# Kernel tuning notes

Measured on AMD Instinct MI355X. Metric: run time of the kernel, lower is better.

Reference implementation:

```python
import jax, jax.numpy as jnp
import numpy as np

# Module config
T = 4.0          # distillation temperature (init arg)
NUM_BINS = 256   # number of unique quantized feature values present in the tensors
N, C, H, W = 64, 256, 32, 32
EPS = 1e-8


def setup_inputs() -> dict:
    key = jax.random.key(0)
    k1, k2 = jax.random.split(key)
    # Quantized features: integer-valued floats in [0, NUM_BINS). All 256 levels
    # appear w.h.p., so torch.unique(features).sort()[0] == arange(NUM_BINS).
    feat_s = jax.random.randint(k1, (N, C, H, W), 0, NUM_BINS).astype(jnp.float32)
    feat_t = jax.random.randint(k2, (N, C, H, W), 0, NUM_BINS).astype(jnp.float32)
    return {"feat_s": feat_s, "feat_t": feat_t}


def _feature_to_prob(features):
    # Replaces the original per-unique-value Python loop with one fused
    # scatter-add histogram. Values are exact integers, so equality-compare
    # counting == bincount on the integer cast.
    b = features.shape[0]
    idx = features.reshape(b, -1).astype(jnp.int32)              # [N, C*H*W]
    hist = jnp.zeros((b, NUM_BINS), jnp.float32)
    hist = hist.at[jnp.arange(b)[:, None], idx].add(1.0)         # [N, NUM_BINS]
    return jnp.log(hist + EPS)


def reference(feat_s, feat_t):
    prob_s = _feature_to_prob(feat_s)
    prob_t = _feature_to_prob(feat_t)
    p_s = jax.nn.log_softmax(prob_s / T, axis=1)                 # log-probs
    p_t = jax.nn.softmax(prob_t / T, axis=1)                     # probs
    # F.kl_div(log_input=p_s, target=p_t, size_average=False) = sum p_t*(log p_t - p_s)
    kl = jnp.sum(p_t * (jnp.log(p_t) - p_s))
    loss = kl * (T ** 2) / feat_s.shape[0]
    return loss
```

## Files before the change

### kernel.cpp

```cpp
#include <hip/hip_runtime.h>

#define NBATCH    64
#define BINS      256
#define PER_BATCH (256 * 32 * 32)
#define THREADS   256
#define CHUNKS    16
#define F4_PER_CHUNK (PER_BATCH / 4 / CHUNKS)
#define F4_PER_THREAD (F4_PER_CHUNK / THREADS)

__global__ __launch_bounds__(THREADS, 5) void hist_kernel(
    const float* __restrict__ fs, const float* __restrict__ ft,
    int* __restrict__ phist) {
  __shared__ unsigned sh[64 * 128];
  const int tid = threadIdx.x;

  uint4* shv = (uint4*)sh;
#pragma unroll
  for (int k = 0; k < 8; ++k) shv[k * THREADS + tid] = make_uint4(0, 0, 0, 0);
  __syncthreads();

  const int tb    = blockIdx.x >> 4;
  const int chunk = blockIdx.x & 15;
  const float* src   = (tb < NBATCH) ? fs : ft;
  const int    batch = tb & (NBATCH - 1);
  const float4* p = (const float4*)(src + (size_t)batch * PER_BATCH)
                    + (size_t)chunk * F4_PER_CHUNK;

  const unsigned colb = ((unsigned)tid >> 1) << 2;

#define PROC1(x) {                                        \
    int b = (int)(x);                                     \
    unsigned a = ((unsigned)(b >> 2) << 9) + colb;        \
    atomicAdd((unsigned*)((char*)sh + a),                 \
              1u << ((b & 3) << 3)); }
#define PROC4(v) { PROC1(v.x) PROC1(v.y) PROC1(v.z) PROC1(v.w) }

  float4 c[8];
#pragma unroll
  for (int k = 0; k < 8; ++k) c[k] = p[k * THREADS + tid];
#pragma unroll
  for (int k = 0; k < 8; ++k) {
    float4 n = p[(8 + k) * THREADS + tid];
    PROC4(c[k])
    c[k] = n;
  }
#pragma unroll
  for (int k = 0; k < 8; ++k) PROC4(c[k])
  __syncthreads();

  const int g = tid >> 2;
  const unsigned qbase = (unsigned)g * 128u + (unsigned)(tid & 3) * 32u;
  unsigned acc0 = 0, acc1 = 0;
#pragma unroll 4
  for (int j = 0; j < 32; ++j) {
    unsigned w = sh[qbase + ((j + tid) & 31)];
    acc0 += w & 0x00FF00FFu;
    acc1 += (w >> 8) & 0x00FF00FFu;
  }
  acc0 += __shfl_xor(acc0, 1);  acc0 += __shfl_xor(acc0, 2);
  acc1 += __shfl_xor(acc1, 1);  acc1 += __shfl_xor(acc1, 2);

  const int sub = tid & 3;
  unsigned cnt = (((sub & 1) ? acc1 : acc0) >> ((sub & 2) * 8)) & 0xFFFFu;
  phist[blockIdx.x * BINS + tid] = (int)cnt;
}

__global__ __launch_bounds__(256) void kl_batch(
    const int* __restrict__ phist, double* __restrict__ partial) {
  __shared__ double reda[4], redb[4];
  const int n = blockIdx.x, tid = threadIdx.x;
  const int w = tid >> 6, lane = tid & 63;

  int hs = 0, ht = 0;
#pragma unroll
  for (int c = 0; c < CHUNKS; ++c) {
    hs += phist[(n * CHUNKS + c) * BINS + tid];
    ht += phist[((NBATCH + n) * CHUNKS + c) * BINS + tid];
  }

  double ls = log((double)hs + 1e-8) * 0.25;
  double lt = log((double)ht + 1e-8) * 0.25;

  double ms = ls, mt = lt;
  for (int off = 32; off; off >>= 1) {
    ms = fmax(ms, __shfl_xor(ms, off));
    mt = fmax(mt, __shfl_xor(mt, off));
  }
  if (lane == 0) { reda[w] = ms; redb[w] = mt; }
  __syncthreads();
  ms = fmax(fmax(reda[0], reda[1]), fmax(reda[2], reda[3]));
  mt = fmax(fmax(redb[0], redb[1]), fmax(redb[2], redb[3]));
  __syncthreads();

  double ss = exp(ls - ms), st = exp(lt - mt);
  for (int off = 32; off; off >>= 1) {
    ss += __shfl_xor(ss, off);
    st += __shfl_xor(st, off);
  }
  if (lane == 0) { reda[w] = ss; redb[w] = st; }
  __syncthreads();
  ss = reda[0] + reda[1] + reda[2] + reda[3];
  st = redb[0] + redb[1] + redb[2] + redb[3];
  const double lse_s = ms + log(ss);
  const double lse_t = mt + log(st);

  const double lpt = lt - lse_t;
  const double lps = ls - lse_s;
  double term = exp(lpt) * (lpt - lps);
  for (int off = 32; off; off >>= 1) term += __shfl_xor(term, off);
  __syncthreads();
  if (lane == 0) reda[w] = term;
  __syncthreads();
  if (tid == 0) partial[n] = reda[0] + reda[1] + reda[2] + reda[3];
}

__global__ __launch_bounds__(64) void finalize(
    const double* __restrict__ partial, float* __restrict__ out) {
  double v = partial[threadIdx.x];
  for (int off = 32; off; off >>= 1) v += __shfl_xor(v, off);
  if (threadIdx.x == 0) out[0] = (float)(v * 0.25);
}

extern "C" void kernel_launch(void* const* d_in, const int* in_sizes, int n_in,
                              void* d_out, int out_size, void* d_ws, size_t ws_size,
                              hipStream_t stream) {
  const float* fs = (const float*)d_in[0];
  const float* ft = (const float*)d_in[1];
  int*    phist   = (int*)d_ws;
  double* partial = (double*)((char*)d_ws + (size_t)128 * CHUNKS * BINS * sizeof(int));

  hist_kernel<<<dim3(128 * CHUNKS), dim3(THREADS), 0, stream>>>(fs, ft, phist);
  kl_batch<<<dim3(NBATCH), dim3(256), 0, stream>>>(phist, partial);
  finalize<<<dim3(1), dim3(64), 0, stream>>>(partial, (float*)d_out);
}
```

Measured before the change: 151.3 us.

## Use per-thread private LDS histogram columns instead of shared atomics

Each of the 256 threads now gets its own column of 64 packed byte-counter words, so LDS doubles to 64 KB. Updates become plain read-modify-write instead of atomicAdd. Within each float4, the four values are checked against each other for the same word group and their increments are merged, so no update is lost when two values share a word. The pipelined load loop is restructured into 4-wide batches, and the reduction now walks 64 words per column. The cost is one block per CU's worth of LDS and more ALU work for the conflict resolution; the packed 8-bit counters still take at most 64 counts per thread.

```diff
diff --git a/kernel.cpp b/kernel.cpp
--- a/kernel.cpp
+++ b/kernel.cpp
@@ -5,18 +5,18 @@
 #define PER_BATCH (256 * 32 * 32)
 #define THREADS   256
 #define CHUNKS    16
-#define F4_PER_CHUNK (PER_BATCH / 4 / CHUNKS)
-#define F4_PER_THREAD (F4_PER_CHUNK / THREADS)
+#define F4_PER_THREAD 16
+#define F4_PER_CHUNK (F4_PER_THREAD * THREADS)
 
-__global__ __launch_bounds__(THREADS, 5) void hist_kernel(
+__global__ __launch_bounds__(THREADS) void hist_kernel(
     const float* __restrict__ fs, const float* __restrict__ ft,
     int* __restrict__ phist) {
-  __shared__ unsigned sh[64 * 128];
+  __shared__ unsigned sh[64 * 256];
   const int tid = threadIdx.x;
 
   uint4* shv = (uint4*)sh;
 #pragma unroll
-  for (int k = 0; k < 8; ++k) shv[k * THREADS + tid] = make_uint4(0, 0, 0, 0);
+  for (int k = 0; k < 16; ++k) shv[k * THREADS + tid] = make_uint4(0, 0, 0, 0);
   __syncthreads();
 
   const int tb    = blockIdx.x >> 4;
@@ -26,34 +26,49 @@
   const float4* p = (const float4*)(src + (size_t)batch * PER_BATCH)
                     + (size_t)chunk * F4_PER_CHUNK;
 
-  const unsigned colb = ((unsigned)tid >> 1) << 2;
+#define PROCQ(v) {                                                          \
+    unsigned b0 = (unsigned)(v).x & 255u, b1 = (unsigned)(v).y & 255u,      \
+             b2 = (unsigned)(v).z & 255u, b3 = (unsigned)(v).w & 255u;      \
+    unsigned g0 = b0 >> 2, g1 = b1 >> 2, g2 = b2 >> 2, g3 = b3 >> 2;        \
+    unsigned i0 = 1u << ((b0 & 3u) << 3), i1 = 1u << ((b1 & 3u) << 3),      \
+             i2 = 1u << ((b2 & 3u) << 3), i3 = 1u << ((b3 & 3u) << 3);      \
+    bool e10 = g1 == g0, e20 = g2 == g0, e21 = g2 == g1;                    \
+    bool e30 = g3 == g0, e31 = g3 == g1, e32 = g3 == g2;                    \
+    unsigned m0 = i0 + (e10 ? i1 : 0u) + (e20 ? i2 : 0u) + (e30 ? i3 : 0u); \
+    unsigned m1 = i1 + ((e21 && !e20) ? i2 : 0u)                            \
+                     + ((e31 && !e30) ? i3 : 0u);                           \
+    unsigned m2 = i2 + ((e32 && !e31 && !e30) ? i3 : 0u);                   \
+    unsigned x0 = (g0 << 8) + (unsigned)tid, x1 = (g1 << 8) + (unsigned)tid,\
+             x2 = (g2 << 8) + (unsigned)tid, x3 = (g3 << 8) + (unsigned)tid;\
+    unsigned u0 = sh[x0], u1 = sh[x1], u2 = sh[x2], u3 = sh[x3];            \
+    unsigned f1 = e10 ? m0 : m1;                                            \
+    unsigned f2 = e20 ? m0 : (e21 ? f1 : m2);                               \
+    unsigned f3 = e30 ? m0 : (e31 ? f1 : (e32 ? f2 : i3));                  \
+    sh[x0] = u0 + m0; sh[x1] = u1 + f1;                                     \
+    sh[x2] = u2 + f2; sh[x3] = u3 + f3; }
 
-#define PROC1(x) {                                        \
-    int b = (int)(x);                                     \
-    unsigned a = ((unsigned)(b >> 2) << 9) + colb;        \
-    atomicAdd((unsigned*)((char*)sh + a),                 \
-              1u << ((b & 3) << 3)); }
-#define PROC4(v) { PROC1(v.x) PROC1(v.y) PROC1(v.z) PROC1(v.w) }
-
-  float4 c[8];
+  float4 c[4];
 #pragma unroll
-  for (int k = 0; k < 8; ++k) c[k] = p[k * THREADS + tid];
+  for (int k = 0; k < 4; ++k) c[k] = p[k * THREADS + tid];
 #pragma unroll
-  for (int k = 0; k < 8; ++k) {
-    float4 n = p[(8 + k) * THREADS + tid];
-    PROC4(c[k])
-    c[k] = n;
+  for (int it = 0; it < 3; ++it) {
+#pragma unroll
+    for (int k = 0; k < 4; ++k) {
+      float4 n = p[((it + 1) * 4 + k) * THREADS + tid];
+      PROCQ(c[k])
+      c[k] = n;
+    }
   }
 #pragma unroll
-  for (int k = 0; k < 8; ++k) PROC4(c[k])
+  for (int k = 0; k < 4; ++k) PROCQ(c[k])
   __syncthreads();
 
   const int g = tid >> 2;
-  const unsigned qbase = (unsigned)g * 128u + (unsigned)(tid & 3) * 32u;
+  const unsigned qbase = (unsigned)g * 256u + (unsigned)(tid & 3) * 64u;
   unsigned acc0 = 0, acc1 = 0;
 #pragma unroll 4
-  for (int j = 0; j < 32; ++j) {
-    unsigned w = sh[qbase + ((j + tid) & 31)];
+  for (int j = 0; j < 64; ++j) {
+    unsigned w = sh[qbase + ((j + tid) & 63)];
     acc0 += w & 0x00FF00FFu;
     acc1 += (w >> 8) & 0x00FF00FFu;
   }
```

New measurement: 155.1 us. 2.5% more time.

## Use private per-thread LDS histogram columns with plain read-modify-write instead of atomics

Applied to the files above, without the earlier changes.

Each thread now owns its own LDS column of packed 8-bit counters, so LDS atomicAdd becomes plain load/add/store. Values are handled in pairs with a same-address check so that two increments to the same word are merged correctly. Block size drops to 128 threads and the chunk count doubles to keep per-thread work the same, and the reduction now sums 128 columns per bin. Non-atomic LDS updates should be cheaper, but the 32 KB LDS per block with only 128 threads limits occupancy and doubles the partial histograms kl_batch must read.

```diff
diff --git a/kernel.cpp b/kernel.cpp
--- a/kernel.cpp
+++ b/kernel.cpp
@@ -3,12 +3,12 @@
 #define NBATCH    64
 #define BINS      256
 #define PER_BATCH (256 * 32 * 32)
-#define THREADS   256
-#define CHUNKS    16
-#define F4_PER_CHUNK (PER_BATCH / 4 / CHUNKS)
-#define F4_PER_THREAD (F4_PER_CHUNK / THREADS)
+#define THREADS   128
+#define CHUNKS    32
+#define F4_PER_THREAD 16
+#define F4_PER_CHUNK (F4_PER_THREAD * THREADS)
 
-__global__ __launch_bounds__(THREADS, 5) void hist_kernel(
+__global__ __launch_bounds__(THREADS) void hist_kernel(
     const float* __restrict__ fs, const float* __restrict__ ft,
     int* __restrict__ phist) {
   __shared__ unsigned sh[64 * 128];
@@ -16,24 +16,33 @@
 
   uint4* shv = (uint4*)sh;
 #pragma unroll
-  for (int k = 0; k < 8; ++k) shv[k * THREADS + tid] = make_uint4(0, 0, 0, 0);
+  for (int k = 0; k < 16; ++k) shv[k * THREADS + tid] = make_uint4(0, 0, 0, 0);
   __syncthreads();
 
-  const int tb    = blockIdx.x >> 4;
-  const int chunk = blockIdx.x & 15;
+  const int tb    = blockIdx.x >> 5;
+  const int chunk = blockIdx.x & 31;
   const float* src   = (tb < NBATCH) ? fs : ft;
   const int    batch = tb & (NBATCH - 1);
   const float4* p = (const float4*)(src + (size_t)batch * PER_BATCH)
                     + (size_t)chunk * F4_PER_CHUNK;
 
-  const unsigned colb = ((unsigned)tid >> 1) << 2;
+  const unsigned colb = (unsigned)tid << 2;
 
-#define PROC1(x) {                                        \
-    int b = (int)(x);                                     \
-    unsigned a = ((unsigned)(b >> 2) << 9) + colb;        \
-    atomicAdd((unsigned*)((char*)sh + a),                 \
-              1u << ((b & 3) << 3)); }
-#define PROC4(v) { PROC1(v.x) PROC1(v.y) PROC1(v.z) PROC1(v.w) }
+#define PAIR(ax, bx) {                                                \
+    unsigned b0 = (unsigned)(ax) & 255u, b1 = (unsigned)(bx) & 255u;  \
+    unsigned a0 = ((b0 & 0xFCu) << 7) + colb;                         \
+    unsigned a1 = ((b1 & 0xFCu) << 7) + colb;                         \
+    unsigned i0 = 1u << ((b0 & 3u) << 3);                             \
+    unsigned i1 = 1u << ((b1 & 3u) << 3);                             \
+    unsigned u0 = *(const unsigned*)((const char*)sh + a0);           \
+    unsigned u1 = *(const unsigned*)((const char*)sh + a1);           \
+    bool e = (a0 == a1);                                              \
+    unsigned m0 = i0 + (e ? i1 : 0u);                                 \
+    unsigned f1 = e ? m0 : i1;                                        \
+    *(unsigned*)((char*)sh + a0) = u0 + m0;                           \
+    *(unsigned*)((char*)sh + a1) = u1 + f1; }
+
+#define PROCQ(v) { PAIR((v).x, (v).y) PAIR((v).z, (v).w) }
 
   float4 c[8];
 #pragma unroll
@@ -41,28 +50,24 @@
 #pragma unroll
   for (int k = 0; k < 8; ++k) {
     float4 n = p[(8 + k) * THREADS + tid];
-    PROC4(c[k])
+    PROCQ(c[k])
     c[k] = n;
   }
 #pragma unroll
-  for (int k = 0; k < 8; ++k) PROC4(c[k])
+  for (int k = 0; k < 8; ++k) PROCQ(c[k])
   __syncthreads();
 
-  const int g = tid >> 2;
-  const unsigned qbase = (unsigned)g * 128u + (unsigned)(tid & 3) * 32u;
-  unsigned acc0 = 0, acc1 = 0;
-#pragma unroll 4
-  for (int j = 0; j < 32; ++j) {
-    unsigned w = sh[qbase + ((j + tid) & 31)];
-    acc0 += w & 0x00FF00FFu;
-    acc1 += (w >> 8) & 0x00FF00FFu;
+  const int l = tid & 63, w = tid >> 6;
+  const unsigned gbase = (unsigned)l * 128u;
+  unsigned acc = 0;
+#pragma unroll 8
+  for (int j = 0; j < 128; ++j) {
+    unsigned word = sh[gbase + ((unsigned)(j + l) & 127u)];
+    acc += (w ? (word >> 8) : word) & 0x00FF00FFu;
   }
-  acc0 += __shfl_xor(acc0, 1);  acc0 += __shfl_xor(acc0, 2);
-  acc1 += __shfl_xor(acc1, 1);  acc1 += __shfl_xor(acc1, 2);
-
-  const int sub = tid & 3;
-  unsigned cnt = (((sub & 1) ? acc1 : acc0) >> ((sub & 2) * 8)) & 0xFFFFu;
-  phist[blockIdx.x * BINS + tid] = (int)cnt;
+  const int obase = blockIdx.x * BINS + 4 * l + w;
+  phist[obase]     = (int)(acc & 0xFFFFu);
+  phist[obase + 2] = (int)(acc >> 16);
 }
 
 __global__ __launch_bounds__(256) void kl_batch(
@@ -72,7 +77,7 @@
   const int w = tid >> 6, lane = tid & 63;
 
   int hs = 0, ht = 0;
-#pragma unroll
+#pragma unroll 8
   for (int c = 0; c < CHUNKS; ++c) {
     hs += phist[(n * CHUNKS + c) * BINS + tid];
     ht += phist[((NBATCH + n) * CHUNKS + c) * BINS + tid];
```

New measurement: 160.2 us. 5.9% more time.
